# Optimization experiments

Hardware: AMD Instinct MI355X
Metric: run time of the kernel (lower is better)

The kernel has to match this reference:

```python
import jax, jax.numpy as jnp
import numpy as np

WS = 8
NH = 16
EPS = 1e-5

# relative position index (static, same as the torch buffer)
def _rel_index(ws):
    coords = np.stack(np.meshgrid(np.arange(ws), np.arange(ws), indexing='ij'))  # 2,ws,ws
    flat = coords.reshape(2, -1)
    rel = flat[:, :, None] - flat[:, None, :]
    rel = rel.transpose(1, 2, 0).copy()
    rel[..., 0] += ws - 1
    rel[..., 1] += ws - 1
    rel[..., 0] *= 2 * ws - 1
    return rel.sum(-1)  # (ws*ws, ws*ws)

REL_IDX = jnp.asarray(_rel_index(WS))

def conv2d(x, w, dilation=1, pad=None, groups=1):
    k = w.shape[-1]
    if pad is None:
        pad = (dilation * (k - 1)) // 2
    return jax.lax.conv_general_dilated(
        x, w, (1, 1), ((pad, pad), (pad, pad)), rhs_dilation=(dilation, dilation),
        dimension_numbers=('NCHW', 'OIHW', 'NCHW'), feature_group_count=groups)

def bn(x, p):
    g, b, m, v = p[0], p[1], p[2], p[3]
    inv = g / jnp.sqrt(v + EPS)
    return x * inv[:, None, None] + (b - m * inv)[:, None, None]

def avgpool(x, kh, kw, ph, pw):
    # torch AvgPool2d with count_include_pad=True: zero-pad then divide by kernel size
    s = jax.lax.reduce_window(x, 0.0, jax.lax.add, (1, 1, kh, kw), (1, 1, 1, 1),
                              ((0, 0), (0, 0), (ph, ph), (pw, pw)))
    return s / (kh * kw)

def _fwd(x, w_pre, bn_pre, w_l1, bn_l1, w_l2, bn_l2, w_l3, bn_l3, w_qkv, rpb, w_dw, w_pw, bn_proj):
    B, C, H, W = x.shape
    # local conv branch (chunk 256 -> 86,86,84 with dilations 1,2,3)
    local = bn(conv2d(x, w_pre), bn_pre)
    l1 = bn(conv2d(local[:, :86], w_l1, dilation=1), bn_l1)
    l2 = bn(conv2d(local[:, 86:172], w_l2, dilation=2), bn_l2)
    l3 = bn(conv2d(local[:, 172:], w_l3, dilation=3), bn_l3)
    local = jnp.concatenate([l1, l2, l3], axis=1)
    # pad to window multiple (reflect); static shapes so Python branch is fine
    ph, pw = (-H) % WS, (-W) % WS
    if ph or pw:
        x = jnp.pad(x, ((0, 0), (0, 0), (0, ph), (0, pw)), mode='reflect')
    Hp, Wp = H + ph, W + pw
    hh, ww = Hp // WS, Wp // WS
    d = C // NH
    qkv = conv2d(x, w_qkv)  # (B, 3C, Hp, Wp)
    qkv = qkv.reshape(B, 3, NH, d, hh, WS, ww, WS)
    qkv = qkv.transpose(1, 0, 4, 6, 2, 5, 7, 3).reshape(3, B * hh * ww, NH, WS * WS, d)
    q, k, v = qkv[0], qkv[1], qkv[2]
    dots = jnp.einsum('whid,whjd->whij', q, k) * (d ** -0.5)
    bias = rpb[REL_IDX.reshape(-1)].reshape(WS * WS, WS * WS, NH).transpose(2, 0, 1)
    attn = jax.nn.softmax(dots + bias[None], axis=-1)
    out = jnp.einsum('whij,whjd->whid', attn, v)
    out = out.reshape(B, hh, ww, NH, WS, WS, d).transpose(0, 3, 6, 1, 4, 2, 5).reshape(B, C, Hp, Wp)
    out = out[:, :, :H, :W]
    ax = avgpool(jnp.pad(out, ((0, 0), (0, 0), (0, 1), (0, 0)), mode='reflect'), WS, 1, WS // 2 - 1, 0)
    ay = avgpool(jnp.pad(out, ((0, 0), (0, 0), (0, 0), (0, 1)), mode='reflect'), 1, WS, 0, WS // 2 - 1)
    out = ax + ay + local
    out = jnp.pad(out, ((0, 0), (0, 0), (0, 1), (0, 1)), mode='reflect')
    out = conv2d(out, w_dw, pad=3, groups=C)       # depthwise 8x8
    out = bn(conv2d(out, w_pw), bn_proj)           # pointwise + BN
    return out[:, :, :H, :W]

def setup_inputs() -> dict:
    key = jax.random.key(0)
    ks = jax.random.split(key, 16)
    def w(k, shape, s=0.05):
        return jax.random.normal(k, shape, dtype=jnp.float32) * s
    def bnp(k, c):
        p = jax.random.uniform(k, (4, c), dtype=jnp.float32)
        return p.at[3].add(0.5)  # keep var positive and away from 0
    return {
        'x': jax.random.normal(ks[0], (8, 256, 128, 128), dtype=jnp.float32),
        'w_pre': w(ks[1], (256, 256, 1, 1)), 'bn_pre': bnp(ks[2], 256),
        'w_l1': w(ks[3], (86, 86, 3, 3)), 'bn_l1': bnp(ks[4], 86),
        'w_l2': w(ks[5], (86, 86, 3, 3)), 'bn_l2': bnp(ks[6], 86),
        'w_l3': w(ks[7], (84, 84, 3, 3)), 'bn_l3': bnp(ks[8], 84),
        'w_qkv': w(ks[9], (768, 256, 1, 1)),
        'rpb': w(ks[10], (225, 16), 0.02),
        'w_dw': w(ks[11], (256, 1, 8, 8)),
        'w_pw': w(ks[12], (256, 256, 1, 1)),
        'bn_proj': bnp(ks[13], 256),
    }

def reference(x, w_pre, bn_pre, w_l1, bn_l1, w_l2, bn_l2, w_l3, bn_l3, w_qkv, rpb, w_dw, w_pw, bn_proj):
    return _fwd(x, w_pre, bn_pre, w_l1, bn_l1, w_l2, bn_l2, w_l3, bn_l3, w_qkv, rpb, w_dw, w_pw, bn_proj)
```

## Files before the change

### kernel.cpp

```cpp
#include <hip/hip_runtime.h>
#include <hip/hip_bf16.h>
#include <cstdint>
#include <cstddef>

namespace {

constexpr int HW = 16384;

typedef short vec8s __attribute__((ext_vector_type(8)));
typedef float f32x4 __attribute__((ext_vector_type(4)));

__device__ __forceinline__ float u2f(uint32_t u){ union { uint32_t u; float f; } v; v.u = u; return v.f; }
__device__ __forceinline__ uint32_t f2u(float f){ union { float f; uint32_t u; } v; v.f = f; return v.u; }
__device__ __forceinline__ uint16_t f2bf(float f){
  uint32_t u = f2u(f);
  u += 0x7fffu + ((u >> 16) & 1u);
  return (uint16_t)(u >> 16);
}
__device__ __forceinline__ void unpack2(uint32_t w, float& lo, float& hi){
  lo = u2f(w << 16);
  hi = u2f(w & 0xffff0000u);
}

__global__ __launch_bounds__(256) void k_w2bf(
    const float* __restrict__ src, uint16_t* __restrict__ dst, int n)
{
  int i = (blockIdx.x * 256 + threadIdx.x) * 8;
  if (i + 8 <= n) {
    float4 a = *(const float4*)(src + i);
    float4 b = *(const float4*)(src + i + 4);
    uint4 pk;
    pk.x = (uint32_t)f2bf(a.x) | ((uint32_t)f2bf(a.y) << 16);
    pk.y = (uint32_t)f2bf(a.z) | ((uint32_t)f2bf(a.w) << 16);
    pk.z = (uint32_t)f2bf(b.x) | ((uint32_t)f2bf(b.y) << 16);
    pk.w = (uint32_t)f2bf(b.z) | ((uint32_t)f2bf(b.w) << 16);
    *(uint4*)(dst + i) = pk;
  }
}

__global__ __launch_bounds__(256) void k_cast(
    const float* __restrict__ x, uint16_t* __restrict__ xT)
{
  __shared__ float sF[64][129];
  const int t = threadIdx.x;
  const int b = blockIdx.x >> 7;
  const int y = blockIdx.x & 127;
  const size_t rowoff = (size_t)y * 128;
  for (int cc = 0; cc < 4; ++cc) {
    const int cic0 = cc * 64;
    #pragma unroll
    for (int k = 0; k < 8; ++k) {
      int e = t + k * 256;
      int ci = e >> 5;
      int pxq = (e & 31) * 4;
      float4 v = *(const float4*)(x + (size_t)(b * 256 + cic0 + ci) * HW + rowoff + pxq);
      sF[ci][pxq] = v.x; sF[ci][pxq+1] = v.y; sF[ci][pxq+2] = v.z; sF[ci][pxq+3] = v.w;
    }
    __syncthreads();
    {
      int px = t >> 1, h = t & 1;
      __align__(16) uint16_t tmp[32];
      #pragma unroll
      for (int j = 0; j < 32; ++j) tmp[j] = f2bf(sF[h * 32 + j][px]);
      uint16_t* dst = xT + ((size_t)b * HW + rowoff + px) * 256 + cic0 + h * 32;
      *(uint4*)(dst)      = *(uint4*)&tmp[0];
      *(uint4*)(dst + 8)  = *(uint4*)&tmp[8];
      *(uint4*)(dst + 16) = *(uint4*)&tmp[16];
      *(uint4*)(dst + 24) = *(uint4*)&tmp[24];
    }
    __syncthreads();
  }
}

template<int OUT_MODE, int NCO>
__global__ __launch_bounds__(256) void k_gemm_v2(
    const uint16_t* __restrict__ xT, const uint16_t* __restrict__ wbf,
    const float* __restrict__ bnp, int M,
    uint16_t* __restrict__ outb, float* __restrict__ outf)
{
  __shared__ __align__(16) uint16_t sX[128][260];
  __shared__ __align__(16) uint16_t sW[128][36];
  const int t = threadIdx.x;
  const int b    = blockIdx.x >> 7;
  const int tile = blockIdx.x & 127;
  const int l = t & 63, w = t >> 6;
  const int l15 = l & 15, koct = l >> 4;
  const int wc = w >> 1, wp = w & 1;

  {
    const int spx = t >> 1, sh = t & 1;
    int gpx;
    if constexpr (OUT_MODE == 3) {
      int win = tile * 2 + (spx >> 6);
      int p = spx & 63;
      gpx = ((win >> 4) * 8 + (p >> 3)) * 128 + (win & 15) * 8 + (p & 7);
    } else {
      gpx = tile * 128 + spx;
    }
    const uint16_t* src = xT + ((size_t)b * HW + gpx) * 256 + sh * 128;
    uint16_t* dst = &sX[spx][sh * 128];
    #pragma unroll
    for (int i = 0; i < 16; ++i)
      *(uint4*)(dst + i * 8) = *(const uint4*)(src + i * 8);
  }

  const int swc = t >> 1, swh = t & 1;
  uint4 wr0, wr1;
  {
    const uint16_t* p = wbf + (size_t)swc * 256 + swh * 16;
    wr0 = *(const uint4*)(p);
    wr1 = *(const uint4*)(p + 8);
  }
  __syncthreads();

  for (int cc = 0; cc < NCO; ++cc) {
    f32x4 acc[4][4];
    #pragma unroll
    for (int cf = 0; cf < 4; ++cf)
      #pragma unroll
      for (int pf = 0; pf < 4; ++pf) acc[cf][pf] = (f32x4){0.f,0.f,0.f,0.f};

    for (int kc = 0; kc < 8; ++kc) {
      if (cc | kc) __syncthreads();
      {
        uint16_t* dst = &sW[swc][swh * 16];
        *(uint4*)(dst)     = wr0;
        *(uint4*)(dst + 8) = wr1;
      }
      {
        int nkc = kc + 1, ncc = cc;
        if (nkc == 8) { nkc = 0; ncc = cc + 1; }
        if (ncc < NCO) {
          const uint16_t* p = wbf + (size_t)(ncc * 128 + swc) * 256 + nkc * 32 + swh * 16;
          wr0 = *(const uint4*)(p);
          wr1 = *(const uint4*)(p + 8);
        }
      }
      __syncthreads();
      vec8s bf[4];
      #pragma unroll
      for (int pf = 0; pf < 4; ++pf)
        bf[pf] = *(const vec8s*)&sX[wp * 64 + pf * 16 + l15][kc * 32 + koct * 8];
      #pragma unroll
      for (int cf = 0; cf < 4; ++cf) {
        vec8s af = *(const vec8s*)&sW[wc * 64 + cf * 16 + l15][koct * 8];
        #pragma unroll
        for (int pf = 0; pf < 4; ++pf)
          acc[cf][pf] = __builtin_amdgcn_mfma_f32_16x16x32_bf16(af, bf[pf], acc[cf][pf], 0, 0, 0);
      }
    }

    #pragma unroll
    for (int cf = 0; cf < 4; ++cf) {
      const int cbase = cc * 128 + wc * 64 + cf * 16 + koct * 4;
      float scv[4], shv[4];
      #pragma unroll
      for (int r = 0; r < 4; ++r) {
        scv[r] = 1.f; shv[r] = 0.f;
        if constexpr (OUT_MODE == 0 || OUT_MODE == 2) {
          int c = cbase + r;
          float g = bnp[c], be = bnp[M + c], mu = bnp[2 * M + c], va = bnp[3 * M + c];
          scv[r] = g * rsqrtf(va + 1e-5f);
          shv[r] = be - mu * scv[r];
        }
      }
      #pragma unroll
      for (int pf = 0; pf < 4; ++pf) {
        if constexpr (OUT_MODE == 0) {
          int px = tile * 128 + wp * 64 + pf * 16 + l15;
          __align__(8) uint16_t pk[4];
          #pragma unroll
          for (int r = 0; r < 4; ++r)
            pk[r] = f2bf(fmaf(acc[cf][pf][r], scv[r], shv[r]));
          *(uint2*)(outb + ((size_t)b * HW + px) * 256 + cbase) = *(uint2*)pk;
        } else if constexpr (OUT_MODE == 2) {
          int px = tile * 128 + wp * 64 + pf * 16 + l15;
          #pragma unroll
          for (int r = 0; r < 4; ++r)
            outf[(size_t)(b * M + cbase + r) * HW + px] =
                fmaf(acc[cf][pf][r], scv[r], shv[r]);
        } else {
          int win = tile * 2 + wp;
          int p = pf * 16 + l15;
          uint16_t* dstp = outb + ((size_t)(b * 256 + win) * 768 + cbase) * 64 + p;
          #pragma unroll
          for (int r = 0; r < 4; ++r)
            dstp[(size_t)r * 64] = f2bf(acc[cf][pf][r]);
        }
      }
    }
  }
}

template<int DIL, int CG>
__global__ __launch_bounds__(256) void k_dilconv_mfma(
    const uint16_t* __restrict__ preT, const float* __restrict__ wt,
    const float* __restrict__ bnp, float* __restrict__ out,
    int cb, int cb_al)
{
  constexpr int R = 8 + 2 * DIL;
  constexpr int C = 64 + 2 * DIL;
  constexpr int NPOS = R * C;
  constexpr int NIT = (NPOS + 255) / 256;
  __shared__ __align__(16) uint16_t sX[NPOS * 16];
  __shared__ __align__(16) uint16_t sW[10 * 50 * 16];

  const int t = threadIdx.x;
  const int rt    = blockIdx.x >> 1;
  const int ctile = blockIdx.x & 1;
  const int ct2   = blockIdx.y;
  const int b     = blockIdx.z;
  const int y0 = rt * 8, x0 = ctile * 64;
  const int l = t & 63, w = t >> 6;
  const int l15 = l & 15, oct = (l >> 4) & 1, half = l >> 5;
  const int rbase = w * 2;

  f32x4 acc[3][8];
  #pragma unroll
  for (int cf = 0; cf < 3; ++cf)
    #pragma unroll
    for (int q = 0; q < 8; ++q) acc[cf][q] = (f32x4){0.f,0.f,0.f,0.f};

  for (int kc = 0; kc < 6; ++kc) {
    #pragma unroll
    for (int i = 0; i < 3; ++i) {
      int pair = t + i * 256;
      int co = pair >> 4, ci = pair & 15;
      int cog = ct2 * 48 + co;
      int c = cb_al + kc * 16 + ci;
      bool ok = (cog < CG) && (c >= cb) && (c < cb + CG);
      size_t widx = ok ? ((size_t)cog * (size_t)CG + (size_t)(c - cb)) * 9u
                       : (size_t)0;
      const float* wp = wt + widx;
      uint16_t* dst = &sW[co * 16 + ci];
      #pragma unroll
      for (int tap = 0; tap < 9; ++tap)
        dst[tap * 800] = ok ? f2bf(wp[tap]) : (uint16_t)0;
      dst[9 * 800] = 0;
    }
    #pragma unroll
    for (int i = 0; i < NIT; ++i) {
      int p = t + i * 256;
      if (p < NPOS) {
        int row = p / C, col = p % C;
        int gy = y0 + row - DIL, gx = x0 + col - DIL;
        uint4 va = {0,0,0,0}, vb = {0,0,0,0};
        if ((unsigned)gy < 128u && (unsigned)gx < 128u) {
          const uint4* src = (const uint4*)(preT +
              (((size_t)b * HW + gy * 128 + gx) * 256 + cb_al + kc * 16));
          va = src[0]; vb = src[1];
        }
        uint4* dst = (uint4*)&sX[p * 16];
        dst[0] = va; dst[1] = vb;
      }
    }
    __syncthreads();

    #pragma unroll
    for (int s = 0; s < 5; ++s) {
      const int tap0 = 2 * s, tap1 = 2 * s + 1;
      const int dy0 = tap0 / 3, dx0 = tap0 % 3;
      const int dy1 = (tap1 <= 8) ? tap1 / 3 : 2;
      const int dx1 = (tap1 <= 8) ? tap1 % 3 : 2;
      const int dy = half ? dy1 : dy0;
      const int dx = half ? dx1 : dx0;
      const int atap = tap0 + half;
      vec8s a0 = *(const vec8s*)&sW[(atap * 50 + 0  + l15) * 16 + oct * 8];
      vec8s a1 = *(const vec8s*)&sW[(atap * 50 + 16 + l15) * 16 + oct * 8];
      vec8s a2 = *(const vec8s*)&sW[(atap * 50 + 32 + l15) * 16 + oct * 8];
      #pragma unroll
      for (int rs = 0; rs < 2; ++rs) {
        const int rowin = rbase + rs + dy * DIL;
        #pragma unroll
        for (int c4 = 0; c4 < 4; ++c4) {
          const int colin = c4 * 16 + l15 + dx * DIL;
          vec8s bf = *(const vec8s*)&sX[(rowin * C + colin) * 16 + oct * 8];
          acc[0][rs*4+c4] = __builtin_amdgcn_mfma_f32_16x16x32_bf16(a0, bf, acc[0][rs*4+c4], 0, 0, 0);
          acc[1][rs*4+c4] = __builtin_amdgcn_mfma_f32_16x16x32_bf16(a1, bf, acc[1][rs*4+c4], 0, 0, 0);
          acc[2][rs*4+c4] = __builtin_amdgcn_mfma_f32_16x16x32_bf16(a2, bf, acc[2][rs*4+c4], 0, 0, 0);
        }
      }
    }
    __syncthreads();
  }

  const int row4 = (l >> 4);
  #pragma unroll
  for (int cf = 0; cf < 3; ++cf) {
    #pragma unroll
    for (int r = 0; r < 4; ++r) {
      int c_loc = ct2 * 48 + cf * 16 + row4 * 4 + r;
      if (c_loc < CG) {
        int cg = cb + c_loc;
        float g = bnp[c_loc], be = bnp[CG + c_loc];
        float mu = bnp[2 * CG + c_loc], va = bnp[3 * CG + c_loc];
        float scv = g * rsqrtf(va + 1e-5f);
        float shv = be - mu * scv;
        #pragma unroll
        for (int rs = 0; rs < 2; ++rs) {
          int y = y0 + rbase + rs;
          #pragma unroll
          for (int c4 = 0; c4 < 4; ++c4) {
            int x = x0 + c4 * 16 + l15;
            out[(size_t)(b * 256 + cg) * HW + y * 128 + x] =
                fmaf(acc[cf][rs*4+c4][r], scv, shv);
          }
        }
      }
    }
  }
}

__global__ __launch_bounds__(256) void k_attn(
    const uint16_t* __restrict__ qkvW, const float* __restrict__ rpb,
    uint16_t* __restrict__ outp)
{
  __shared__ __align__(16) uint16_t sAll[4][9928];
  const int t = threadIdx.x;
  const int l = t & 63, w = t >> 6;
  const int l15 = l & 15, koct = l >> 4;
  const int b = blockIdx.y;
  const int win = blockIdx.x;
  const int wy = win >> 4, wx = win & 15;
  const int wbase = (wy * 8) * 128 + wx * 8;
  const uint16_t* base = qkvW + (size_t)(b * 256 + win) * 49152;
  uint16_t* swKT = &sAll[w][0];
  uint16_t* swQT = &sAll[w][2560];
  uint16_t* swPT = &sAll[w][5120];
  float*    swB  = (float*)&sAll[w][9472];
  float*    swO  = (float*)swPT;

  {
    uint4 z = {0,0,0,0};
    *(uint4*)(swKT + l * 40 + 16) = z;
    *(uint4*)(swKT + l * 40 + 24) = z;
    *(uint4*)(swQT + l * 40 + 16) = z;
    *(uint4*)(swQT + l * 40 + 24) = z;
  }

  for (int it = 0; it < 4; ++it) {
    const int n = w + it * 4;
    #pragma unroll
    for (int m = 0; m < 4; ++m) {
      int e = l + m * 64;
      if (e < 225) swB[e] = rpb[e * 16 + n];
    }
    const uint16_t* qg = base + (size_t)(n * 16) * 64;
    const uint16_t* kg = base + (size_t)(256 + n * 16) * 64;
    const uint16_t* vg = base + (size_t)(512 + n * 16) * 64;
    {
      uint32_t kp[8], qp[8];
      #pragma unroll
      for (int m = 0; m < 8; ++m) {
        uint32_t k0 = kg[(2 * m) * 64 + l], k1 = kg[(2 * m + 1) * 64 + l];
        uint32_t q0 = qg[(2 * m) * 64 + l], q1 = qg[(2 * m + 1) * 64 + l];
        kp[m] = k0 | (k1 << 16);
        qp[m] = q0 | (q1 << 16);
      }
      *(uint4*)(swKT + l * 40)     = *(uint4*)&kp[0];
      *(uint4*)(swKT + l * 40 + 8) = *(uint4*)&kp[4];
      *(uint4*)(swQT + l * 40)     = *(uint4*)&qp[0];
      *(uint4*)(swQT + l * 40 + 8) = *(uint4*)&qp[4];
    }
    asm volatile("s_waitcnt lgkmcnt(0)" ::: "memory");
    __builtin_amdgcn_sched_barrier(0);

    vec8s aK[4], bQ[4];
    #pragma unroll
    for (int tt = 0; tt < 4; ++tt) {
      aK[tt] = *(const vec8s*)(swKT + (tt * 16 + l15) * 40 + koct * 8);
      bQ[tt] = *(const vec8s*)(swQT + (tt * 16 + l15) * 40 + koct * 8);
    }
    f32x4 accS[4][4];
    #pragma unroll
    for (int ti = 0; ti < 4; ++ti)
      #pragma unroll
      for (int tj = 0; tj < 4; ++tj)
        accS[ti][tj] = __builtin_amdgcn_mfma_f32_16x16x32_bf16(
            aK[tj], bQ[ti], (f32x4){0.f, 0.f, 0.f, 0.f}, 0, 0, 0);

    float p[4][16], sinv[4];
    #pragma unroll
    for (int ti = 0; ti < 4; ++ti) {
      const int i = ti * 16 + l15;
      const int irow = i >> 3, icol = i & 7;
      #pragma unroll
      for (int tj = 0; tj < 4; ++tj) {
        #pragma unroll
        for (int r = 0; r < 4; ++r) {
          int j = tj * 16 + koct * 4 + r;
          int rel = (irow - (j >> 3) + 7) * 15 + (icol - (j & 7) + 7);
          p[ti][tj * 4 + r] = fmaf(accS[ti][tj][r], 0.25f, swB[rel]);
        }
      }
      float mx = p[ti][0];
      #pragma unroll
      for (int u = 1; u < 16; ++u) mx = fmaxf(mx, p[ti][u]);
      mx = fmaxf(mx, __shfl_xor(mx, 16));
      mx = fmaxf(mx, __shfl_xor(mx, 32));
      float s = 0.f;
      #pragma unroll
      for (int u = 0; u < 16; ++u) { p[ti][u] = __expf(p[ti][u] - mx); s += p[ti][u]; }
      s += __shfl_xor(s, 16);
      s += __shfl_xor(s, 32);
      sinv[ti] = 1.f / s;
    }

    #pragma unroll
    for (int ti = 0; ti < 4; ++ti) {
      uint16_t* rowp = swPT + (ti * 16 + l15) * 68 + koct * 4;
      #pragma unroll
      for (int tj = 0; tj < 4; ++tj) {
        uint32_t u0 = (uint32_t)f2bf(p[ti][tj * 4 + 0]) | ((uint32_t)f2bf(p[ti][tj * 4 + 1]) << 16);
        uint32_t u1 = (uint32_t)f2bf(p[ti][tj * 4 + 2]) | ((uint32_t)f2bf(p[ti][tj * 4 + 3]) << 16);
        *(uint32_t*)(rowp + tj * 16)     = u0;
        *(uint32_t*)(rowp + tj * 16 + 2) = u1;
      }
    }
    asm volatile("s_waitcnt lgkmcnt(0)" ::: "memory");
    __builtin_amdgcn_sched_barrier(0);

    f32x4 accO[4];
    #pragma unroll
    for (int ii = 0; ii < 4; ++ii) accO[ii] = (f32x4){0.f, 0.f, 0.f, 0.f};
    #pragma unroll
    for (int ks = 0; ks < 2; ++ks) {
      vec8s aV = *(const vec8s*)(vg + l15 * 64 + ks * 32 + koct * 8);
      #pragma unroll
      for (int ii = 0; ii < 4; ++ii) {
        vec8s bP;
        const uint16_t* src = swPT + (ii * 16 + l15) * 68 + ks * 32 + koct * 8;
        *(uint2*)&bP         = *(const uint2*)(src);
        *((uint2*)&bP + 1)   = *(const uint2*)(src + 4);
        accO[ii] = __builtin_amdgcn_mfma_f32_16x16x32_bf16(aV, bP, accO[ii], 0, 0, 0);
      }
    }
    asm volatile("s_waitcnt lgkmcnt(0)" ::: "memory");
    __builtin_amdgcn_sched_barrier(0);

    #pragma unroll
    for (int ii = 0; ii < 4; ++ii) {
      #pragma unroll
      for (int r = 0; r < 4; ++r) {
        int dd = koct * 4 + r;
        swO[dd * 76 + ii * 16 + l15] = accO[ii][r] * sinv[ii];
      }
    }
    asm volatile("s_waitcnt lgkmcnt(0)" ::: "memory");
    __builtin_amdgcn_sched_barrier(0);
    #pragma unroll
    for (int e2 = 0; e2 < 2; ++e2) {
      int e = l + e2 * 64;
      int dd = e >> 3, row = e & 7;
      const float* orow = swO + dd * 76 + row * 8;
      float4 a = *(const float4*)(orow);
      float4 c = *(const float4*)(orow + 4);
      uint4 pk;
      pk.x = (uint32_t)f2bf(a.x) | ((uint32_t)f2bf(a.y) << 16);
      pk.y = (uint32_t)f2bf(a.z) | ((uint32_t)f2bf(a.w) << 16);
      pk.z = (uint32_t)f2bf(c.x) | ((uint32_t)f2bf(c.y) << 16);
      pk.w = (uint32_t)f2bf(c.z) | ((uint32_t)f2bf(c.w) << 16);
      *(uint4*)(outp + (size_t)(b * 256 + n * 16 + dd) * HW + wbase + row * 128) = pk;
    }
    asm volatile("s_waitcnt lgkmcnt(0)" ::: "memory");
    __builtin_amdgcn_sched_barrier(0);
  }
}

__global__ __launch_bounds__(256) void k_pool(
    const uint16_t* __restrict__ attnb, float* __restrict__ loc)
{
  __shared__ __align__(16) float sP[71][136];
  const int t = threadIdx.x;
  const int plane = blockIdx.x >> 1;
  const int h0 = (blockIdx.x & 1) * 64;
  const size_t pbase = (size_t)plane * HW;
  #pragma unroll
  for (int k = 0; k < 5; ++k) {
    int idx = t + k * 256;
    if (idx < 71 * 16) {
      int lr = idx >> 4, m = idx & 15;
      int g = h0 - 3 + lr;
      float f[8] = {0.f,0.f,0.f,0.f,0.f,0.f,0.f,0.f};
      if (g >= 0 && g <= 127) {
        uint4 v4 = *(const uint4*)(attnb + pbase + (size_t)g * 128 + m * 8);
        unpack2(v4.x, f[0], f[1]); unpack2(v4.y, f[2], f[3]);
        unpack2(v4.z, f[4], f[5]); unpack2(v4.w, f[6], f[7]);
      }
      float* dst = &sP[lr][4 + m * 8];
      *(float4*)dst       = (float4){f[0], f[1], f[2], f[3]};
      *(float4*)(dst + 4) = (float4){f[4], f[5], f[6], f[7]};
    }
  }
  #pragma unroll
  for (int k = 0; k < 3; ++k) {
    int idx = t + k * 256;
    if (idx < 71 * 8) {
      int lr = idx >> 3, e = idx & 7;
      int c = (e < 4) ? e : (128 + e);
      sP[lr][c] = 0.f;
    }
  }
  __syncthreads();

  const int q  = t & 31;
  const int r0 = (t >> 5) * 8;
  const int w0 = q * 4;
  float4 av = {0.f, 0.f, 0.f, 0.f};
  #pragma unroll
  for (int o = 0; o < 8; ++o) {
    float4 v = *(const float4*)&sP[r0 + o][4 + w0];
    av.x += v.x; av.y += v.y; av.z += v.z; av.w += v.w;
  }
  #pragma unroll
  for (int rr = 0; rr < 8; ++rr) {
    const int lh = r0 + rr;
    const int h = h0 + lh;
    float4 a = av;
    if (h >= 124) {
      float4 cfix = *(const float4*)&sP[126 - 64 + 3][4 + w0];
      a.x += cfix.x; a.y += cfix.y; a.z += cfix.z; a.w += cfix.w;
    }
    float4 hv0 = *(const float4*)&sP[lh + 3][w0];
    float4 hv1 = *(const float4*)&sP[lh + 3][w0 + 4];
    float4 hv2 = *(const float4*)&sP[lh + 3][w0 + 8];
    float s0 = hv0.y + hv0.z + hv0.w + hv1.x + hv1.y + hv1.z + hv1.w + hv2.x;
    float s1 = s0 - hv0.y + hv2.y;
    float s2 = s1 - hv0.z + hv2.z;
    float s3 = s2 - hv0.w + hv2.w;
    if (q == 31) {
      float cfix = sP[lh + 3][130];
      s0 += cfix; s1 += cfix; s2 += cfix; s3 += cfix;
    }
    const size_t gi = pbase + (size_t)h * 128 + w0;
    float4 lv = *(const float4*)(loc + gi);
    float4 o4;
    o4.x = fmaf(a.x + s0, 0.125f, lv.x);
    o4.y = fmaf(a.y + s1, 0.125f, lv.y);
    o4.z = fmaf(a.z + s2, 0.125f, lv.z);
    o4.w = fmaf(a.w + s3, 0.125f, lv.w);
    *(float4*)(loc + gi) = o4;
    if (rr < 7) {
      float4 vm = *(const float4*)&sP[lh][4 + w0];
      float4 vp = *(const float4*)&sP[lh + 8][4 + w0];
      av.x += vp.x - vm.x; av.y += vp.y - vm.y;
      av.z += vp.z - vm.z; av.w += vp.w - vm.w;
    }
  }
}

__global__ __launch_bounds__(256) void k_dw(
    const float* __restrict__ comb, const float* __restrict__ wdw,
    float* __restrict__ out)
{
  __shared__ __align__(16) float sZ[71][136];
  __shared__ float sWd[64];
  const int t = threadIdx.x;
  const int plane = blockIdx.x >> 1;
  const int cch = plane & 255;
  const int h0 = (blockIdx.x & 1) * 64;
  const size_t pbase = (size_t)plane * HW;
  if (t < 64) sWd[t] = wdw[cch * 64 + t];
  #pragma unroll
  for (int k = 0; k < 5; ++k) {
    int idx = t + k * 256;
    if (idx < 71 * 16) {
      int lr = idx >> 4, m = idx & 15;
      int g = h0 - 3 + lr;
      float4 a = {0.f,0.f,0.f,0.f}, c = {0.f,0.f,0.f,0.f};
      if (g >= 0 && g <= 128) {
        int gr = (g == 128) ? 126 : g;
        const float* src = comb + pbase + (size_t)gr * 128 + m * 8;
        a = *(const float4*)(src);
        c = *(const float4*)(src + 4);
      }
      float* dst = &sZ[lr][4 + m * 8];
      *(float4*)dst       = a;
      *(float4*)(dst + 4) = c;
    }
  }
  if (t < 71) {
    int lr = t;
    int g = h0 - 3 + lr;
    float rv = 0.f;
    if (g >= 0 && g <= 128) {
      int gr = (g == 128) ? 126 : g;
      rv = comb[pbase + (size_t)gr * 128 + 126];
    }
    *(float4*)&sZ[lr][0] = (float4){0.f, 0.f, 0.f, 0.f};
    sZ[lr][132] = rv;
    sZ[lr][133] = 0.f; sZ[lr][134] = 0.f; sZ[lr][135] = 0.f;
  }
  __syncthreads();

  float wt[8][8];
  #pragma unroll
  for (int i = 0; i < 8; ++i) {
    *(float4*)&wt[i][0] = *(const float4*)&sWd[i * 8];
    *(float4*)&wt[i][4] = *(const float4*)&sWd[i * 8 + 4];
  }

  const int q  = t & 31;
  const int rg = t >> 5;
  const int w0 = q * 4;
  f32x4 acc[8];
  #pragma unroll
  for (int rr = 0; rr < 8; ++rr) acc[rr] = (f32x4){0.f,0.f,0.f,0.f};

  #pragma unroll
  for (int v = 0; v < 15; ++v) {
    const int lr = rg * 8 + v;
    float win[12];
    *(float4*)&win[0] = *(const float4*)&sZ[lr][w0];
    *(float4*)&win[4] = *(const float4*)&sZ[lr][w0 + 4];
    *(float4*)&win[8] = *(const float4*)&sZ[lr][w0 + 8];
    #pragma unroll
    for (int rr = 0; rr < 8; ++rr) {
      const int i = v - rr;
      if (i >= 0 && i < 8) {
        #pragma unroll
        for (int c = 0; c < 4; ++c) {
          float s = acc[rr][c];
          #pragma unroll
          for (int j = 0; j < 8; ++j)
            s = fmaf(wt[i][j], win[c + j + 1], s);
          acc[rr][c] = s;
        }
      }
    }
  }
  #pragma unroll
  for (int rr = 0; rr < 8; ++rr) {
    int h = h0 + rg * 8 + rr;
    float* dst = out + pbase + (size_t)h * 128 + w0;
    *(float4*)dst = (float4){acc[rr][0], acc[rr][1], acc[rr][2], acc[rr][3]};
  }
}

}

extern "C" void kernel_launch(void* const* d_in, const int* in_sizes, int n_in,
                              void* d_out, int out_size, void* d_ws, size_t ws_size,
                              hipStream_t stream)
{
  const float* x      = (const float*)d_in[0];
  const float* w_pre  = (const float*)d_in[1];
  const float* bn_pre = (const float*)d_in[2];
  const float* w_l1   = (const float*)d_in[3];
  const float* bn_l1  = (const float*)d_in[4];
  const float* w_l2   = (const float*)d_in[5];
  const float* bn_l2  = (const float*)d_in[6];
  const float* w_l3   = (const float*)d_in[7];
  const float* bn_l3  = (const float*)d_in[8];
  const float* w_qkv  = (const float*)d_in[9];
  const float* rpb    = (const float*)d_in[10];
  const float* w_dw   = (const float*)d_in[11];
  const float* w_pw   = (const float*)d_in[12];
  const float* bn_pj  = (const float*)d_in[13];
  float* out = (float*)d_out;

  char* base = (char*)d_ws;
  uint16_t* xT    = (uint16_t*)base;
  uint16_t* preT  = (uint16_t*)(base + (size_t)67108864);
  float*    bufB  = (float*)(base + (size_t)134217728);
  uint16_t* bufQ  = (uint16_t*)(base + (size_t)268435456);
  uint16_t* attnO = preT;
  float*    bufDw = (float*)bufQ;
  uint16_t* dwT   = xT;
  uint16_t* wpre_bf = (uint16_t*)out;
  uint16_t* wqkv_bf = wpre_bf + 65536;
  uint16_t* wpw_bf  = preT;

  dim3 blk(256);
  k_w2bf<<<dim3(32),  blk, 0, stream>>>(w_pre, wpre_bf, 65536);
  k_w2bf<<<dim3(96),  blk, 0, stream>>>(w_qkv, wqkv_bf, 196608);
  k_cast<<<dim3(1024), blk, 0, stream>>>(x, xT);
  k_gemm_v2<0, 2><<<dim3(1024), blk, 0, stream>>>(xT, wpre_bf, bn_pre, 256, preT, nullptr);
  k_dilconv_mfma<1, 86><<<dim3(32, 2, 8), blk, 0, stream>>>(preT, w_l1, bn_l1, bufB, 0, 0);
  k_dilconv_mfma<2, 86><<<dim3(32, 2, 8), blk, 0, stream>>>(preT, w_l2, bn_l2, bufB, 86, 80);
  k_dilconv_mfma<3, 84><<<dim3(32, 2, 8), blk, 0, stream>>>(preT, w_l3, bn_l3, bufB, 172, 160);
  k_gemm_v2<3, 6><<<dim3(1024), blk, 0, stream>>>(xT, wqkv_bf, nullptr, 768, bufQ, nullptr);
  k_attn<<<dim3(256, 8), blk, 0, stream>>>(bufQ, rpb, attnO);
  k_pool<<<dim3(4096), blk, 0, stream>>>(attnO, bufB);
  k_w2bf<<<dim3(32), blk, 0, stream>>>(w_pw, wpw_bf, 65536);
  k_dw<<<dim3(4096), blk, 0, stream>>>(bufB, w_dw, bufDw);
  k_cast<<<dim3(1024), blk, 0, stream>>>(bufDw, dwT);
  k_gemm_v2<2, 2><<<dim3(1024), blk, 0, stream>>>(dwT, wpw_bf, bn_pj, 256, nullptr, out);

  (void)in_sizes; (void)n_in; (void)out_size; (void)ws_size;
}
```

Baseline: 729.7 us.

## Prefetch next head's Q/K/rpb into registers and alias P buffer onto K/Q LDS

The attention kernel now loads the next head's Q, K and relative-position-bias values into registers while the current head is being computed. It also issues the V loads early, before the softmax. The P/output scratch now reuses the K/Q LDS region, which cuts per-block shared memory roughly in half and should allow higher occupancy. The cost is more live registers and re-zeroing the padding each iteration, because the P writes overwrite the K/Q area.

```diff
diff --git a/kernel.cpp b/kernel.cpp
--- a/kernel.cpp
+++ b/kernel.cpp
@@ -315,7 +315,7 @@
     const uint16_t* __restrict__ qkvW, const float* __restrict__ rpb,
     uint16_t* __restrict__ outp)
 {
-  __shared__ __align__(16) uint16_t sAll[4][9928];
+  __shared__ __align__(16) uint16_t sAll[4][5632];
   const int t = threadIdx.x;
   const int l = t & 63, w = t >> 6;
   const int l15 = l & 15, koct = l >> 4;
@@ -326,16 +326,26 @@
   const uint16_t* base = qkvW + (size_t)(b * 256 + win) * 49152;
   uint16_t* swKT = &sAll[w][0];
   uint16_t* swQT = &sAll[w][2560];
-  uint16_t* swPT = &sAll[w][5120];
-  float*    swB  = (float*)&sAll[w][9472];
-  float*    swO  = (float*)swPT;
-
-  {
-    uint4 z = {0,0,0,0};
-    *(uint4*)(swKT + l * 40 + 16) = z;
-    *(uint4*)(swKT + l * 40 + 24) = z;
-    *(uint4*)(swQT + l * 40 + 16) = z;
-    *(uint4*)(swQT + l * 40 + 24) = z;
+  uint16_t* swPT = &sAll[w][0];
+  float*    swO  = (float*)&sAll[w][0];
+  float*    swB  = (float*)&sAll[w][5120];
+
+  const uint16_t* qg = base + (size_t)(w * 16) * 64;
+  const uint16_t* kg = qg + 256 * 64;
+  const uint16_t* vg = qg + 512 * 64;
+  uint32_t kp[8], qp[8];
+  float breg[4];
+  #pragma unroll
+  for (int m = 0; m < 8; ++m) {
+    uint32_t k0 = kg[(2 * m) * 64 + l], k1 = kg[(2 * m + 1) * 64 + l];
+    uint32_t q0 = qg[(2 * m) * 64 + l], q1 = qg[(2 * m + 1) * 64 + l];
+    kp[m] = k0 | (k1 << 16);
+    qp[m] = q0 | (q1 << 16);
+  }
+  #pragma unroll
+  for (int m = 0; m < 4; ++m) {
+    int e = l + m * 64;
+    breg[m] = (e < 225) ? rpb[e * 16 + w] : 0.f;
   }
 
   for (int it = 0; it < 4; ++it) {
@@ -343,24 +353,36 @@
     #pragma unroll
     for (int m = 0; m < 4; ++m) {
       int e = l + m * 64;
-      if (e < 225) swB[e] = rpb[e * 16 + n];
-    }
-    const uint16_t* qg = base + (size_t)(n * 16) * 64;
-    const uint16_t* kg = base + (size_t)(256 + n * 16) * 64;
-    const uint16_t* vg = base + (size_t)(512 + n * 16) * 64;
+      if (e < 225) swB[e] = breg[m];
+    }
     {
-      uint32_t kp[8], qp[8];
+      uint4 z = {0, 0, 0, 0};
+      *(uint4*)(swKT + l * 40)      = *(uint4*)&kp[0];
+      *(uint4*)(swKT + l * 40 + 8)  = *(uint4*)&kp[4];
+      *(uint4*)(swKT + l * 40 + 16) = z;
+      *(uint4*)(swKT + l * 40 + 24) = z;
+      *(uint4*)(swQT + l * 40)      = *(uint4*)&qp[0];
+      *(uint4*)(swQT + l * 40 + 8)  = *(uint4*)&qp[4];
+      *(uint4*)(swQT + l * 40 + 16) = z;
+      *(uint4*)(swQT + l * 40 + 24) = z;
+    }
+    vec8s vA0 = *(const vec8s*)(vg + l15 * 64 + koct * 8);
+    vec8s vA1 = *(const vec8s*)(vg + l15 * 64 + 32 + koct * 8);
+    if (it < 3) {
+      const uint16_t* qg2 = qg + 4096;
+      const uint16_t* kg2 = kg + 4096;
       #pragma unroll
       for (int m = 0; m < 8; ++m) {
-        uint32_t k0 = kg[(2 * m) * 64 + l], k1 = kg[(2 * m + 1) * 64 + l];
-        uint32_t q0 = qg[(2 * m) * 64 + l], q1 = qg[(2 * m + 1) * 64 + l];
+        uint32_t k0 = kg2[(2 * m) * 64 + l], k1 = kg2[(2 * m + 1) * 64 + l];
+        uint32_t q0 = qg2[(2 * m) * 64 + l], q1 = qg2[(2 * m + 1) * 64 + l];
         kp[m] = k0 | (k1 << 16);
         qp[m] = q0 | (q1 << 16);
       }
-      *(uint4*)(swKT + l * 40)     = *(uint4*)&kp[0];
-      *(uint4*)(swKT + l * 40 + 8) = *(uint4*)&kp[4];
-      *(uint4*)(swQT + l * 40)     = *(uint4*)&qp[0];
-      *(uint4*)(swQT + l * 40 + 8) = *(uint4*)&qp[4];
+      #pragma unroll
+      for (int m = 0; m < 4; ++m) {
+        int e = l + m * 64;
+        breg[m] = (e < 225) ? rpb[e * 16 + n + 4] : 0.f;
+      }
     }
     asm volatile("s_waitcnt lgkmcnt(0)" ::: "memory");
     __builtin_amdgcn_sched_barrier(0);
@@ -425,13 +447,13 @@
     for (int ii = 0; ii < 4; ++ii) accO[ii] = (f32x4){0.f, 0.f, 0.f, 0.f};
     #pragma unroll
     for (int ks = 0; ks < 2; ++ks) {
-      vec8s aV = *(const vec8s*)(vg + l15 * 64 + ks * 32 + koct * 8);
+      vec8s aV = ks ? vA1 : vA0;
       #pragma unroll
       for (int ii = 0; ii < 4; ++ii) {
         vec8s bP;
         const uint16_t* src = swPT + (ii * 16 + l15) * 68 + ks * 32 + koct * 8;
-        *(uint2*)&bP         = *(const uint2*)(src);
-        *((uint2*)&bP + 1)   = *(const uint2*)(src + 4);
+        *(uint2*)&bP       = *(const uint2*)(src);
+        *((uint2*)&bP + 1) = *(const uint2*)(src + 4);
         accO[ii] = __builtin_amdgcn_mfma_f32_16x16x32_bf16(aV, bP, accO[ii], 0, 0, 0);
       }
     }
@@ -464,6 +486,7 @@
     }
     asm volatile("s_waitcnt lgkmcnt(0)" ::: "memory");
     __builtin_amdgcn_sched_barrier(0);
+    qg += 4096; kg += 4096; vg += 4096;
   }
 }
 
```

Result: no change. 720.2 us (-1.3%).
